# Kernel optimization log

Hardware: AMD Instinct MI355X
Metric: run time of the kernel (lower is better)

The kernel has to match this reference:

```python
import jax, jax.numpy as jnp
import numpy as np

ALPHA = 0.4
EPS = float(np.finfo(np.float32).eps)  # torch.finfo(fp32).eps
BATCH, VOCAB, RANK = 256, 128000, 64


def setup_inputs() -> dict:
    key = jax.random.key(0)
    k1, k2, k3 = jax.random.split(key, 3)
    token_ids = jax.random.randint(k1, (BATCH, 1), 0, VOCAB, dtype=jnp.int64 if jax.config.jax_enable_x64 else jnp.int32)
    logits = jax.random.normal(k2, (BATCH, VOCAB), dtype=jnp.float32)
    W = jax.random.normal(k3, (VOCAB, RANK), dtype=jnp.float32)
    return {"token_ids": token_ids, "logits": logits, "W": W}


def reference(token_ids, logits, W):
    # _rescaled_mint_no_cast (remove_basis=True):
    #   Lp_raw = L @ W @ W.T - L   (low-rank mint, basis removed)
    Lp_raw = (logits @ W) @ W.T - logits  # [B, V]
    # Guarantee max|L'| <= max|L| via global abs-max rescale.
    scale = jnp.max(jnp.abs(logits)) / jnp.maximum(jnp.max(jnp.abs(Lp_raw)), EPS)
    minted = Lp_raw * scale
    # Modes.Lerp: torch.lerp(minted, logits, alpha) = minted + alpha*(logits - minted)
    return minted + ALPHA * (logits - minted)
```

## Files before the change

kernel.cpp:

```cpp
#include <hip/hip_runtime.h>
#include <math.h>

#define ALPHA_F 0.4f
#define FP32_EPS 1.1920928955078125e-7f
#define NB 256
#define NV 128000
#define NR 64

typedef _Float16 half_t;
typedef _Float16 half2_t __attribute__((ext_vector_type(2)));
typedef _Float16 half4_t __attribute__((ext_vector_type(4)));
typedef _Float16 half8 __attribute__((ext_vector_type(8)));
typedef float f32x4 __attribute__((ext_vector_type(4)));


__global__ __launch_bounds__(256) void k0_prep(const float* __restrict__ W,
                                               half_t* __restrict__ Wg,
                                               half_t* __restrict__ Wf,
                                               float* __restrict__ P,
                                               unsigned* __restrict__ maxbits) {
    __shared__ half_t tile[256 * 72];
    const int t  = threadIdx.x;
    const int k0 = blockIdx.x * 256;

    if (blockIdx.x < 64) P[blockIdx.x * 256 + t] = 0.f;
    if (blockIdx.x == 0 && t < 2) maxbits[t] = 0u;

#pragma unroll
    for (int i = 0; i < 16; ++i) {
        const int f  = i * 256 + t;
        const int kr = f >> 4;
        const int n4 = (f & 15) * 4;
        const float4 v = *(const float4*)(W + (size_t)(k0 + kr) * NR + n4);
        half2_t h01 = { (half_t)v.x, (half_t)v.y };
        half2_t h23 = { (half_t)v.z, (half_t)v.w };
        *(half2_t*)&tile[kr * 72 + n4]     = h01;
        *(half2_t*)&tile[kr * 72 + n4 + 2] = h23;
    }
    __syncthreads();

#pragma unroll
    for (int i = 0; i < 8; ++i) {
        const int idx  = i * 256 + t;
        const int kk_l = idx >> 8;
        const int rem  = idx & 255;
        const int nt   = rem >> 6;
        const int lane = rem & 63;
        const int q = lane >> 4, il = lane & 15;
        half8 v;
#pragma unroll
        for (int j = 0; j < 8; ++j)
            v[j] = tile[(kk_l * 32 + q * 8 + j) * 72 + nt * 16 + il];
        const int kt = blockIdx.x * 8 + kk_l;
        *(half8*)(Wg + ((size_t)(kt * 4 + nt) * 64 + lane) * 8) = v;
    }

    if (Wf) {
#pragma unroll
        for (int i = 0; i < 8; ++i) {
            const int idx  = i * 256 + t;
            const int vt_l = idx >> 7;
            const int ks   = (idx >> 6) & 1;
            const int lane = idx & 63;
            const int q = lane >> 4, il = lane & 15;
            half8 v = *(const half8*)&tile[(vt_l * 16 + il) * 72 + ks * 32 + q * 8];
            const int vt = blockIdx.x * 16 + vt_l;
            *(half8*)(Wf + ((size_t)(vt * 2 + ks) * 64 + lane) * 8) = v;
        }
    }
}

__global__ __launch_bounds__(256) void k1_pmm(const float* __restrict__ L,
                                              const half_t* __restrict__ Wg,
                                              float* __restrict__ Ppart,
                                              half_t* __restrict__ Lh,
                                              unsigned* __restrict__ maxbits) {
    __shared__ char lds[64 * 512];
    __shared__ float red[4];
    const int t  = threadIdx.x;
    const int l  = t & 63;
    const int w  = t >> 6;
    const int q  = l >> 4;
    const int il = l & 15;
    const int chunk = blockIdx.x;
    const int mq    = blockIdx.y;
    const int row0  = mq * 64;
    const int col0  = chunk * 256;

    float amax = 0.f;

    {
        const int tr = t >> 5;
        const int tc = t & 31;
#pragma unroll
        for (int p = 0; p < 8; ++p) {
            const int r = p * 8 + tr;
            const size_t g = (size_t)(row0 + r) * NV + col0 + tc * 8;
            const float4 f0 = *(const float4*)(L + g);
            const float4 f1 = *(const float4*)(L + g + 4);
            amax = fmaxf(amax, fmaxf(fmaxf(fabsf(f0.x), fabsf(f0.y)),
                                     fmaxf(fabsf(f0.z), fabsf(f0.w))));
            amax = fmaxf(amax, fmaxf(fmaxf(fabsf(f1.x), fabsf(f1.y)),
                                     fmaxf(fabsf(f1.z), fabsf(f1.w))));
            half8 h = { (half_t)f0.x, (half_t)f0.y, (half_t)f0.z, (half_t)f0.w,
                        (half_t)f1.x, (half_t)f1.y, (half_t)f1.z, (half_t)f1.w };
            if (Lh) *(half8*)(Lh + g) = h;
            const int off = r * 512 + ((tc * 16) ^ (tr << 4));
            *(half8*)(lds + off) = h;
        }
    }
    __syncthreads();

    f32x4 acc[4] = {};
    const int arow = w * 16 + il;
    const int abase = arow * 512;
    const int axor  = (il & 7) << 4;
#pragma unroll
    for (int ks = 0; ks < 8; ++ks) {
        const int kt = chunk * 8 + ks;
        half8 b[4];
#pragma unroll
        for (int nt = 0; nt < 4; ++nt)
            b[nt] = *(const half8*)(Wg + ((size_t)(kt * 4 + nt) * 64 + l) * 8);
        const half8 a = *(const half8*)(lds + ((abase + ks * 64 + q * 16) ^ axor));
#pragma unroll
        for (int nt = 0; nt < 4; ++nt)
            acc[nt] = __builtin_amdgcn_mfma_f32_16x16x32_f16(a, b[nt], acc[nt], 0, 0, 0);
    }

    float* pb = Ppart + (size_t)(chunk * 4 + mq) * 4096;
#pragma unroll
    for (int nt = 0; nt < 4; ++nt)
#pragma unroll
        for (int i = 0; i < 4; ++i)
            pb[(w * 16 + q * 4 + i) * 64 + nt * 16 + il] = acc[nt][i];

#pragma unroll
    for (int off = 32; off > 0; off >>= 1)
        amax = fmaxf(amax, __shfl_xor(amax, off, 64));
    if (l == 0) red[w] = amax;
    __syncthreads();
    if (threadIdx.x == 0) {
        float m = fmaxf(fmaxf(red[0], red[1]), fmaxf(red[2], red[3]));
        atomicMax(&maxbits[0], __float_as_uint(m));
    }
}

__global__ __launch_bounds__(256) void k1b_reduce(const float* __restrict__ Ppart,
                                                  float* __restrict__ P) {
    const int g  = blockIdx.x * 256 + threadIdx.x;
    const int M  = g >> 6, n = g & 63;
    const int mq = M >> 6, r = M & 63;
    const float* p = Ppart + ((size_t)(blockIdx.y * 100) * 4 + mq) * 4096 + r * 64 + n;
    float s = 0.f;
#pragma unroll 4
    for (int c = 0; c < 100; ++c) s += p[(size_t)c * 4 * 4096];
    atomicAdd(&P[g], s);
}

template <bool FAST, bool IS_OUT>
__global__ __launch_bounds__(256) void k23(const float* __restrict__ L,
                                           const half_t* __restrict__ Lh,
                                           const float* __restrict__ W,
                                           const half_t* __restrict__ Wf,
                                           const float* __restrict__ P,
                                           unsigned* __restrict__ maxbits,
                                           float* __restrict__ out) {
    __shared__ float T[64 * 132];
    __shared__ float red[4];
    const int l  = threadIdx.x & 63;
    const int w  = threadIdx.x >> 6;
    const int q  = l >> 4;
    const int il = l & 15;
    const int nc = blockIdx.x;
    const int mq = blockIdx.y;

    half8 a[4][2];
#pragma unroll
    for (int mt = 0; mt < 4; ++mt)
#pragma unroll
        for (int ks = 0; ks < 2; ++ks) {
            const float* pp = P + (size_t)(mq * 64 + mt * 16 + il) * NR + ks * 32 + q * 8;
            const float4 f0 = *(const float4*)pp;
            const float4 f1 = *(const float4*)(pp + 4);
            a[mt][ks] = { (half_t)f0.x, (half_t)f0.y, (half_t)f0.z, (half_t)f0.w,
                          (half_t)f1.x, (half_t)f1.y, (half_t)f1.z, (half_t)f1.w };
        }
#pragma unroll
    for (int ntl = 0; ntl < 2; ++ntl) {
        const int vt = nc * 8 + w * 2 + ntl;
        half8 b[2];
        if (FAST) {
#pragma unroll
            for (int ks = 0; ks < 2; ++ks)
                b[ks] = *(const half8*)(Wf + ((size_t)(vt * 2 + ks) * 64 + l) * 8);
        } else {
#pragma unroll
            for (int ks = 0; ks < 2; ++ks) {
                const float* wp = W + (size_t)(vt * 16 + il) * NR + ks * 32 + q * 8;
                const float4 f0 = *(const float4*)wp;
                const float4 f1 = *(const float4*)(wp + 4);
                b[ks] = { (half_t)f0.x, (half_t)f0.y, (half_t)f0.z, (half_t)f0.w,
                          (half_t)f1.x, (half_t)f1.y, (half_t)f1.z, (half_t)f1.w };
            }
        }
#pragma unroll
        for (int mt = 0; mt < 4; ++mt) {
            f32x4 acc = {};
            acc = __builtin_amdgcn_mfma_f32_16x16x32_f16(a[mt][0], b[0], acc, 0, 0, 0);
            acc = __builtin_amdgcn_mfma_f32_16x16x32_f16(a[mt][1], b[1], acc, 0, 0, 0);
#pragma unroll
            for (int i = 0; i < 4; ++i)
                T[(mt * 16 + q * 4 + i) * 132 + w * 32 + ntl * 16 + il] = acc[i];
        }
    }
    __syncthreads();

    float c1 = 0.f, mx = 0.f;
    if (IS_OUT) {
        const float maxL  = __uint_as_float(maxbits[0]);
        const float maxLp = fmaxf(__uint_as_float(maxbits[1]), FP32_EPS);
        c1 = (1.f - ALPHA_F) * (maxL / maxLp);
    }
#pragma unroll
    for (int i = 0; i < 8; ++i) {
        const int e = i * 1024 + threadIdx.x * 4;
        const int r = e >> 7, c = e & 127;
        const size_t gaddr = (size_t)(mq * 64 + r) * NV + nc * 128 + c;
        const float4 tv = *(const float4*)&T[r * 132 + c];
        float4 lv;
        if (FAST) {
            const half4_t lh = *(const half4_t*)(Lh + gaddr);
            lv = make_float4((float)lh[0], (float)lh[1], (float)lh[2], (float)lh[3]);
        } else {
            lv = *(const float4*)(L + gaddr);
        }
        if (IS_OUT) {
            float4 o;
            o.x = fmaf(c1, tv.x - lv.x, ALPHA_F * lv.x);
            o.y = fmaf(c1, tv.y - lv.y, ALPHA_F * lv.y);
            o.z = fmaf(c1, tv.z - lv.z, ALPHA_F * lv.z);
            o.w = fmaf(c1, tv.w - lv.w, ALPHA_F * lv.w);
            *(float4*)(out + gaddr) = o;
        } else {
            mx = fmaxf(mx, fmaxf(fmaxf(fabsf(tv.x - lv.x), fabsf(tv.y - lv.y)),
                                 fmaxf(fabsf(tv.z - lv.z), fabsf(tv.w - lv.w))));
        }
    }
    if (!IS_OUT) {
#pragma unroll
        for (int off = 32; off > 0; off >>= 1)
            mx = fmaxf(mx, __shfl_xor(mx, off, 64));
        if (l == 0) red[w] = mx;
        __syncthreads();
        if (threadIdx.x == 0) {
            float m = fmaxf(fmaxf(red[0], red[1]), fmaxf(red[2], red[3]));
            atomicMax(&maxbits[1], __float_as_uint(m));
        }
    }
}

extern "C" void kernel_launch(void* const* d_in, const int* in_sizes, int n_in,
                              void* d_out, int out_size, void* d_ws, size_t ws_size,
                              hipStream_t stream) {
    const float* L = (const float*)d_in[1];
    const float* W = (const float*)d_in[2];
    float* out = (float*)d_out;

    unsigned* maxbits = (unsigned*)d_ws;
    float*    P       = (float*)((char*)d_ws + 256);

    const bool fast = ws_size >= (size_t)140 * 1024 * 1024;
    float* Ppart; half_t* Wg; half_t* Wf; half_t* Lh;
    char* ws = (char*)d_ws;
    if (fast) {
        Ppart = (float*)(ws + ((size_t)1  << 20));
        Wg    = (half_t*)(ws + ((size_t)34 << 20));
        Wf    = (half_t*)(ws + ((size_t)51 << 20));
        Lh    = (half_t*)(ws + ((size_t)68 << 20));
    } else {
        Ppart = (float*)d_out;
        Wg    = (half_t*)((char*)d_out + ((size_t)33 << 20));
        Wf    = nullptr;
        Lh    = nullptr;
    }

    k0_prep   <<<500,           256, 0, stream>>>(W, Wg, Wf, P, maxbits);
    k1_pmm    <<<dim3(500, 4),  256, 0, stream>>>(L, Wg, Ppart, Lh, maxbits);
    k1b_reduce<<<dim3(64, 5),   256, 0, stream>>>(Ppart, P);
    if (fast) {
        k23<true,  false><<<dim3(1000, 4), 256, 0, stream>>>(L, Lh, W, Wf, P, maxbits, out);
        k23<true,  true ><<<dim3(1000, 4), 256, 0, stream>>>(L, Lh, W, Wf, P, maxbits, out);
    } else {
        k23<false, false><<<dim3(1000, 4), 256, 0, stream>>>(L, Lh, W, Wf, P, maxbits, out);
        k23<false, true ><<<dim3(1000, 4), 256, 0, stream>>>(L, Lh, W, Wf, P, maxbits, out);
    }
}
```

Measured before the change: 370.4 us.

## Shrink tiles and LDS footprint across kernels to raise occupancy

Halves the per-block work in the prep, the second GEMM/epilogue kernels and the reduce, doubling grid sizes and adding launch_bounds min-blocks hints. In k1_pmm, the A tile is staged in two 128-column halves with a smaller LDS buffer and a barrier between them, so more blocks can be resident per CU. The aim is more in-flight memory traffic on this bandwidth-bound pipeline, at the cost of more blocks, extra barriers, less reuse of the P fragment per block, and more atomics in the reduce.

```diff
diff --git a/kernel.cpp b/kernel.cpp
--- a/kernel.cpp
+++ b/kernel.cpp
@@ -14,20 +14,20 @@
 typedef float f32x4 __attribute__((ext_vector_type(4)));
 
 
-__global__ __launch_bounds__(256) void k0_prep(const float* __restrict__ W,
-                                               half_t* __restrict__ Wg,
-                                               half_t* __restrict__ Wf,
-                                               float* __restrict__ P,
-                                               unsigned* __restrict__ maxbits) {
-    __shared__ half_t tile[256 * 72];
+__global__ __launch_bounds__(256, 8) void k0_prep(const float* __restrict__ W,
+                                                  half_t* __restrict__ Wg,
+                                                  half_t* __restrict__ Wf,
+                                                  float* __restrict__ P,
+                                                  unsigned* __restrict__ maxbits) {
+    __shared__ half_t tile[128 * 72];
     const int t  = threadIdx.x;
-    const int k0 = blockIdx.x * 256;
+    const int k0 = blockIdx.x * 128;
 
     if (blockIdx.x < 64) P[blockIdx.x * 256 + t] = 0.f;
     if (blockIdx.x == 0 && t < 2) maxbits[t] = 0u;
 
 #pragma unroll
-    for (int i = 0; i < 16; ++i) {
+    for (int i = 0; i < 8; ++i) {
         const int f  = i * 256 + t;
         const int kr = f >> 4;
         const int n4 = (f & 15) * 4;
@@ -40,7 +40,7 @@
     __syncthreads();
 
 #pragma unroll
-    for (int i = 0; i < 8; ++i) {
+    for (int i = 0; i < 4; ++i) {
         const int idx  = i * 256 + t;
         const int kk_l = idx >> 8;
         const int rem  = idx & 255;
@@ -51,31 +51,31 @@
 #pragma unroll
         for (int j = 0; j < 8; ++j)
             v[j] = tile[(kk_l * 32 + q * 8 + j) * 72 + nt * 16 + il];
-        const int kt = blockIdx.x * 8 + kk_l;
+        const int kt = blockIdx.x * 4 + kk_l;
         *(half8*)(Wg + ((size_t)(kt * 4 + nt) * 64 + lane) * 8) = v;
     }
 
     if (Wf) {
 #pragma unroll
-        for (int i = 0; i < 8; ++i) {
+        for (int i = 0; i < 4; ++i) {
             const int idx  = i * 256 + t;
             const int vt_l = idx >> 7;
             const int ks   = (idx >> 6) & 1;
             const int lane = idx & 63;
             const int q = lane >> 4, il = lane & 15;
             half8 v = *(const half8*)&tile[(vt_l * 16 + il) * 72 + ks * 32 + q * 8];
-            const int vt = blockIdx.x * 16 + vt_l;
+            const int vt = blockIdx.x * 8 + vt_l;
             *(half8*)(Wf + ((size_t)(vt * 2 + ks) * 64 + lane) * 8) = v;
         }
     }
 }
 
-__global__ __launch_bounds__(256) void k1_pmm(const float* __restrict__ L,
-                                              const half_t* __restrict__ Wg,
-                                              float* __restrict__ Ppart,
-                                              half_t* __restrict__ Lh,
-                                              unsigned* __restrict__ maxbits) {
-    __shared__ char lds[64 * 512];
+__global__ __launch_bounds__(256, 8) void k1_pmm(const float* __restrict__ L,
+                                                 const half_t* __restrict__ Wg,
+                                                 float* __restrict__ Ppart,
+                                                 half_t* __restrict__ Lh,
+                                                 unsigned* __restrict__ maxbits) {
+    __shared__ char lds[64 * 256];
     __shared__ float red[4];
     const int t  = threadIdx.x;
     const int l  = t & 63;
@@ -88,44 +88,43 @@
     const int col0  = chunk * 256;
 
     float amax = 0.f;
-
-    {
-        const int tr = t >> 5;
-        const int tc = t & 31;
+    f32x4 acc[4] = {};
+    const int arow  = w * 16 + il;
+    const int abase = arow * 256;
+    const int axor  = (arow & 7) << 4;
+    const int tr = t >> 5;
+    const int tc = t & 31;
+
+#pragma unroll
+    for (int hh = 0; hh < 2; ++hh) {
+        if (hh) __syncthreads();
+
 #pragma unroll
         for (int p = 0; p < 8; ++p) {
             const int r = p * 8 + tr;
-            const size_t g = (size_t)(row0 + r) * NV + col0 + tc * 8;
+            const size_t g = (size_t)(row0 + r) * NV + col0 + hh * 128 + tc * 4;
             const float4 f0 = *(const float4*)(L + g);
-            const float4 f1 = *(const float4*)(L + g + 4);
             amax = fmaxf(amax, fmaxf(fmaxf(fabsf(f0.x), fabsf(f0.y)),
                                      fmaxf(fabsf(f0.z), fabsf(f0.w))));
-            amax = fmaxf(amax, fmaxf(fmaxf(fabsf(f1.x), fabsf(f1.y)),
-                                     fmaxf(fabsf(f1.z), fabsf(f1.w))));
-            half8 h = { (half_t)f0.x, (half_t)f0.y, (half_t)f0.z, (half_t)f0.w,
-                        (half_t)f1.x, (half_t)f1.y, (half_t)f1.z, (half_t)f1.w };
-            if (Lh) *(half8*)(Lh + g) = h;
-            const int off = r * 512 + ((tc * 16) ^ (tr << 4));
-            *(half8*)(lds + off) = h;
-        }
-    }
-    __syncthreads();
-
-    f32x4 acc[4] = {};
-    const int arow = w * 16 + il;
-    const int abase = arow * 512;
-    const int axor  = (il & 7) << 4;
-#pragma unroll
-    for (int ks = 0; ks < 8; ++ks) {
-        const int kt = chunk * 8 + ks;
-        half8 b[4];
-#pragma unroll
-        for (int nt = 0; nt < 4; ++nt)
-            b[nt] = *(const half8*)(Wg + ((size_t)(kt * 4 + nt) * 64 + l) * 8);
-        const half8 a = *(const half8*)(lds + ((abase + ks * 64 + q * 16) ^ axor));
-#pragma unroll
-        for (int nt = 0; nt < 4; ++nt)
-            acc[nt] = __builtin_amdgcn_mfma_f32_16x16x32_f16(a, b[nt], acc[nt], 0, 0, 0);
+            half4_t h = { (half_t)f0.x, (half_t)f0.y, (half_t)f0.z, (half_t)f0.w };
+            if (Lh) *(half4_t*)(Lh + g) = h;
+            const int off = r * 256 + ((tc * 8) ^ (tr << 4));
+            *(half4_t*)(lds + off) = h;
+        }
+        __syncthreads();
+
+#pragma unroll
+        for (int ksl = 0; ksl < 4; ++ksl) {
+            const int kt = chunk * 8 + hh * 4 + ksl;
+            half8 b[4];
+#pragma unroll
+            for (int nt = 0; nt < 4; ++nt)
+                b[nt] = *(const half8*)(Wg + ((size_t)(kt * 4 + nt) * 64 + l) * 8);
+            const half8 a = *(const half8*)(lds + (abase + ((ksl * 64 + q * 16) ^ axor)));
+#pragma unroll
+            for (int nt = 0; nt < 4; ++nt)
+                acc[nt] = __builtin_amdgcn_mfma_f32_16x16x32_f16(a, b[nt], acc[nt], 0, 0, 0);
+        }
     }
 
     float* pb = Ppart + (size_t)(chunk * 4 + mq) * 4096;
@@ -151,22 +150,22 @@
     const int g  = blockIdx.x * 256 + threadIdx.x;
     const int M  = g >> 6, n = g & 63;
     const int mq = M >> 6, r = M & 63;
-    const float* p = Ppart + ((size_t)(blockIdx.y * 100) * 4 + mq) * 4096 + r * 64 + n;
+    const float* p = Ppart + ((size_t)(blockIdx.y * 25) * 4 + mq) * 4096 + r * 64 + n;
     float s = 0.f;
-#pragma unroll 4
-    for (int c = 0; c < 100; ++c) s += p[(size_t)c * 4 * 4096];
+#pragma unroll 5
+    for (int c = 0; c < 25; ++c) s += p[(size_t)c * 4 * 4096];
     atomicAdd(&P[g], s);
 }
 
 template <bool FAST, bool IS_OUT>
-__global__ __launch_bounds__(256) void k23(const float* __restrict__ L,
-                                           const half_t* __restrict__ Lh,
-                                           const float* __restrict__ W,
-                                           const half_t* __restrict__ Wf,
-                                           const float* __restrict__ P,
-                                           unsigned* __restrict__ maxbits,
-                                           float* __restrict__ out) {
-    __shared__ float T[64 * 132];
+__global__ __launch_bounds__(256, 8) void k23(const float* __restrict__ L,
+                                              const half_t* __restrict__ Lh,
+                                              const float* __restrict__ W,
+                                              const half_t* __restrict__ Wf,
+                                              const float* __restrict__ P,
+                                              unsigned* __restrict__ maxbits,
+                                              float* __restrict__ out) {
+    __shared__ float T[64 * 68];
     __shared__ float red[4];
     const int l  = threadIdx.x & 63;
     const int w  = threadIdx.x >> 6;
@@ -175,44 +174,39 @@
     const int nc = blockIdx.x;
     const int mq = blockIdx.y;
 
-    half8 a[4][2];
-#pragma unroll
-    for (int mt = 0; mt < 4; ++mt)
+    const int vt = nc * 4 + w;
+    half8 b[2];
+    if (FAST) {
+#pragma unroll
+        for (int ks = 0; ks < 2; ++ks)
+            b[ks] = *(const half8*)(Wf + ((size_t)(vt * 2 + ks) * 64 + l) * 8);
+    } else {
+#pragma unroll
+        for (int ks = 0; ks < 2; ++ks) {
+            const float* wp = W + (size_t)(vt * 16 + il) * NR + ks * 32 + q * 8;
+            const float4 f0 = *(const float4*)wp;
+            const float4 f1 = *(const float4*)(wp + 4);
+            b[ks] = { (half_t)f0.x, (half_t)f0.y, (half_t)f0.z, (half_t)f0.w,
+                      (half_t)f1.x, (half_t)f1.y, (half_t)f1.z, (half_t)f1.w };
+        }
+    }
+#pragma unroll
+    for (int mt = 0; mt < 4; ++mt) {
+        half8 a[2];
 #pragma unroll
         for (int ks = 0; ks < 2; ++ks) {
             const float* pp = P + (size_t)(mq * 64 + mt * 16 + il) * NR + ks * 32 + q * 8;
             const float4 f0 = *(const float4*)pp;
             const float4 f1 = *(const float4*)(pp + 4);
-            a[mt][ks] = { (half_t)f0.x, (half_t)f0.y, (half_t)f0.z, (half_t)f0.w,
-                          (half_t)f1.x, (half_t)f1.y, (half_t)f1.z, (half_t)f1.w };
-        }
-#pragma unroll
-    for (int ntl = 0; ntl < 2; ++ntl) {
-        const int vt = nc * 8 + w * 2 + ntl;
-        half8 b[2];
-        if (FAST) {
-#pragma unroll
-            for (int ks = 0; ks < 2; ++ks)
-                b[ks] = *(const half8*)(Wf + ((size_t)(vt * 2 + ks) * 64 + l) * 8);
-        } else {
-#pragma unroll
-            for (int ks = 0; ks < 2; ++ks) {
-                const float* wp = W + (size_t)(vt * 16 + il) * NR + ks * 32 + q * 8;
-                const float4 f0 = *(const float4*)wp;
-                const float4 f1 = *(const float4*)(wp + 4);
-                b[ks] = { (half_t)f0.x, (half_t)f0.y, (half_t)f0.z, (half_t)f0.w,
-                          (half_t)f1.x, (half_t)f1.y, (half_t)f1.z, (half_t)f1.w };
-            }
-        }
-#pragma unroll
-        for (int mt = 0; mt < 4; ++mt) {
-            f32x4 acc = {};
-            acc = __builtin_amdgcn_mfma_f32_16x16x32_f16(a[mt][0], b[0], acc, 0, 0, 0);
-            acc = __builtin_amdgcn_mfma_f32_16x16x32_f16(a[mt][1], b[1], acc, 0, 0, 0);
-#pragma unroll
-            for (int i = 0; i < 4; ++i)
-                T[(mt * 16 + q * 4 + i) * 132 + w * 32 + ntl * 16 + il] = acc[i];
-        }
+            a[ks] = { (half_t)f0.x, (half_t)f0.y, (half_t)f0.z, (half_t)f0.w,
+                      (half_t)f1.x, (half_t)f1.y, (half_t)f1.z, (half_t)f1.w };
+        }
+        f32x4 acc = {};
+        acc = __builtin_amdgcn_mfma_f32_16x16x32_f16(a[0], b[0], acc, 0, 0, 0);
+        acc = __builtin_amdgcn_mfma_f32_16x16x32_f16(a[1], b[1], acc, 0, 0, 0);
+#pragma unroll
+        for (int i = 0; i < 4; ++i)
+            T[(mt * 16 + q * 4 + i) * 68 + w * 16 + il] = acc[i];
     }
     __syncthreads();
 
@@ -223,11 +217,11 @@
         c1 = (1.f - ALPHA_F) * (maxL / maxLp);
     }
 #pragma unroll
-    for (int i = 0; i < 8; ++i) {
+    for (int i = 0; i < 4; ++i) {
         const int e = i * 1024 + threadIdx.x * 4;
-        const int r = e >> 7, c = e & 127;
-        const size_t gaddr = (size_t)(mq * 64 + r) * NV + nc * 128 + c;
-        const float4 tv = *(const float4*)&T[r * 132 + c];
+        const int r = e >> 6, c = e & 63;
+        const size_t gaddr = (size_t)(mq * 64 + r) * NV + nc * 64 + c;
+        const float4 tv = *(const float4*)&T[r * 68 + c];
         float4 lv;
         if (FAST) {
             const half4_t lh = *(const half4_t*)(Lh + gaddr);
@@ -285,14 +279,14 @@
         Lh    = nullptr;
     }
 
-    k0_prep   <<<500,           256, 0, stream>>>(W, Wg, Wf, P, maxbits);
+    k0_prep   <<<1000,          256, 0, stream>>>(W, Wg, Wf, P, maxbits);
     k1_pmm    <<<dim3(500, 4),  256, 0, stream>>>(L, Wg, Ppart, Lh, maxbits);
-    k1b_reduce<<<dim3(64, 5),   256, 0, stream>>>(Ppart, P);
+    k1b_reduce<<<dim3(64, 20),  256, 0, stream>>>(Ppart, P);
     if (fast) {
-        k23<true,  false><<<dim3(1000, 4), 256, 0, stream>>>(L, Lh, W, Wf, P, maxbits, out);
-        k23<true,  true ><<<dim3(1000, 4), 256, 0, stream>>>(L, Lh, W, Wf, P, maxbits, out);
+        k23<true,  false><<<dim3(2000, 4), 256, 0, stream>>>(L, Lh, W, Wf, P, maxbits, out);
+        k23<true,  true ><<<dim3(2000, 4), 256, 0, stream>>>(L, Lh, W, Wf, P, maxbits, out);
     } else {
-        k23<false, false><<<dim3(1000, 4), 256, 0, stream>>>(L, Lh, W, Wf, P, maxbits, out);
-        k23<false, true ><<<dim3(1000, 4), 256, 0, stream>>>(L, Lh, W, Wf, P, maxbits, out);
-    }
-}
+        k23<false, false><<<dim3(2000, 4), 256, 0, stream>>>(L, Lh, W, Wf, P, maxbits, out);
+        k23<false, true ><<<dim3(2000, 4), 256, 0, stream>>>(L, Lh, W, Wf, P, maxbits, out);
+    }
+}
```

New measurement: 520.2 us. 1.4x slower.
